# Kernel optimization log

Hardware: AMD Instinct MI355X
Metric: run time of the kernel (lower is better)

## Reference

```python
import jax, jax.numpy as jnp
import numpy as np

B, T, D_MODEL = 1, 2048, 2048
N_HEADS, N_KV_HEADS, HEAD_DIM = 32, 8, 64
N_REP = N_HEADS // N_KV_HEADS
ROPE_THETA = 10000.0


def setup_inputs() -> dict:
    key = jax.random.key(0)
    ks = jax.random.split(key, 5)
    x = jax.random.normal(ks[0], (B, T, D_MODEL), dtype=jnp.float32)
    # rotary frequencies: complex exp stored as (cos, sin) pairs -> [T, HEAD_DIM//2, 2]
    inv_freq = 1.0 / (ROPE_THETA ** (jnp.arange(0, HEAD_DIM, 2, dtype=jnp.float32) / HEAD_DIM))
    angles = jnp.arange(T, dtype=jnp.float32)[:, None] * inv_freq[None, :]  # [T, HEAD_DIM//2]
    freqs_cis = jnp.stack([jnp.cos(angles), jnp.sin(angles)], axis=-1)  # [T, HD/2, 2]
    s = 1.0 / np.sqrt(D_MODEL)
    wq = jax.random.normal(ks[1], (D_MODEL, N_HEADS * HEAD_DIM), dtype=jnp.float32) * s
    wk = jax.random.normal(ks[2], (D_MODEL, N_KV_HEADS * HEAD_DIM), dtype=jnp.float32) * s
    wv = jax.random.normal(ks[3], (D_MODEL, N_KV_HEADS * HEAD_DIM), dtype=jnp.float32) * s
    wo = jax.random.normal(ks[4], (N_HEADS * HEAD_DIM, D_MODEL), dtype=jnp.float32) * (1.0 / np.sqrt(N_HEADS * HEAD_DIM))
    return {"x": x, "freqs_cis": freqs_cis, "wq": wq, "wk": wk, "wv": wv, "wo": wo}


def _apply_rotary(t, freqs_cis):
    # t: [B, T, H, D]; freqs_cis: [T, D//2, 2] as (cos, sin). Complex multiply.
    tr = t.astype(jnp.float32).reshape(*t.shape[:-1], -1, 2)  # [B,T,H,D/2,2]
    re, im = tr[..., 0], tr[..., 1]
    cos = freqs_cis[None, :, None, :, 0]  # [1,T,1,D/2]
    sin = freqs_cis[None, :, None, :, 1]
    out_re = re * cos - im * sin
    out_im = re * sin + im * cos
    out = jnp.stack([out_re, out_im], axis=-1).reshape(t.shape)
    return out.astype(t.dtype)


def reference(x, freqs_cis, wq, wk, wv, wo):
    Bx, Tx, _ = x.shape
    q = (x @ wq).reshape(Bx, Tx, N_HEADS, HEAD_DIM)
    k = (x @ wk).reshape(Bx, Tx, N_KV_HEADS, HEAD_DIM)
    v = (x @ wv).reshape(Bx, Tx, N_KV_HEADS, HEAD_DIM)
    q = _apply_rotary(q, freqs_cis)
    k = _apply_rotary(k, freqs_cis)
    # GQA: group query heads, broadcast against kv heads (no repeat materialization)
    qg = q.transpose(0, 2, 1, 3).reshape(Bx, N_KV_HEADS, N_REP, Tx, HEAD_DIM)  # [B,G,R,T,D]
    kg = k.transpose(0, 2, 1, 3)  # [B,G,T,D]
    vg = v.transpose(0, 2, 1, 3)  # [B,G,T,D]
    scale = 1.0 / np.sqrt(HEAD_DIM)
    scores = jnp.einsum('bgrtd,bgsd->bgrts', qg, kg) * scale  # [B,G,R,T,T]
    causal = jnp.tril(jnp.ones((Tx, Tx), dtype=bool))
    scores = jnp.where(causal, scores, jnp.finfo(scores.dtype).min)
    p = jax.nn.softmax(scores, axis=-1)
    y = jnp.einsum('bgrts,bgsd->bgrtd', p, vg)  # [B,G,R,T,D]
    y = y.reshape(Bx, N_HEADS, Tx, HEAD_DIM).transpose(0, 2, 1, 3).reshape(Bx, Tx, N_HEADS * HEAD_DIM)
    return y @ wo
```

## Files before the change

kernel.cpp:

```cpp
#include <hip/hip_runtime.h>
#include <hip/hip_bf16.h>
#include <stdint.h>
#include <stddef.h>

#define T_SEQ 2048
#define DMODEL 2048
#define NHEADS 32
#define NKV 8
#define HD 64
#define NQD (NHEADS * HD)
#define NKVD (NKV * HD)
#define QKVN (NQD + 2 * NKVD)

typedef __bf16 bf16_t;
typedef __bf16 bf16x8 __attribute__((ext_vector_type(8)));
typedef __bf16 bf16x4 __attribute__((ext_vector_type(4)));
typedef __bf16 bf16x2 __attribute__((ext_vector_type(2)));
typedef float f32x4 __attribute__((ext_vector_type(4)));

typedef __attribute__((address_space(1))) void gvoid_t;
typedef __attribute__((address_space(3))) void lvoid_t;

__device__ __forceinline__ void gload_lds16(const void* g, void* l) {
  __builtin_amdgcn_global_load_lds((gvoid_t*)g, (lvoid_t*)l, 16, 0, 0);
}

__global__ __launch_bounds__(256) void cast_f32_bf16_kernel(
    const float* __restrict__ in, bf16_t* __restrict__ out, int n8) {
  int i = blockIdx.x * 256 + threadIdx.x;
  if (i >= n8) return;
  const float4* p = (const float4*)in + (size_t)i * 2;
  float4 a = p[0], b = p[1];
  bf16x8 o = {(bf16_t)a.x, (bf16_t)a.y, (bf16_t)a.z, (bf16_t)a.w,
              (bf16_t)b.x, (bf16_t)b.y, (bf16_t)b.z, (bf16_t)b.w};
  *(bf16x8*)(out + (size_t)i * 8) = o;
}

__global__ __launch_bounds__(256) void transpose_cast_kernel(
    const float* __restrict__ in, bf16_t* __restrict__ out,
    int R, int C, int ldin, int ldout) {
  __shared__ float tile[32][33];
  const int c0 = blockIdx.x * 32, r0 = blockIdx.y * 32;
  const int tx = threadIdx.x & 31, ty = threadIdx.x >> 5;
#pragma unroll
  for (int i = 0; i < 32; i += 8)
    tile[ty + i][tx] = in[(size_t)(r0 + ty + i) * ldin + c0 + tx];
  __syncthreads();
#pragma unroll
  for (int i = 0; i < 32; i += 8)
    out[(size_t)(c0 + ty + i) * ldout + r0 + tx] = (bf16_t)tile[tx][ty + i];
}

__global__ __launch_bounds__(256) void rope_cast_kernel(
    const float* __restrict__ src, const float* __restrict__ fc,
    bf16_t* __restrict__ dst, int H, int ldin, float oscale) {
  const int i = blockIdx.x * 256 + threadIdx.x;
  const int npr = H * 32;
  const int t = i / npr;
  const int rem = i - t * npr;
  const int h = rem >> 5, fi = rem & 31;
  const float2 rein = *(const float2*)&src[(size_t)t * ldin + h * 64 + fi * 2];
  const float2 cs = *(const float2*)&fc[((size_t)t * 32 + fi) * 2];
  const float o0 = (rein.x * cs.x - rein.y * cs.y) * oscale;
  const float o1 = (rein.x * cs.y + rein.y * cs.x) * oscale;
  bf16x2 ob = {(bf16_t)o0, (bf16_t)o1};
  *(bf16x2*)&dst[(size_t)t * (H * 64) + h * 64 + fi * 2] = ob;
}

__global__ __launch_bounds__(256) void gemm_bt64_kernel(
    const bf16_t* __restrict__ A, const bf16_t* __restrict__ BT,
    float* __restrict__ C, int M, int N, int K) {
  __shared__ bf16_t As[2][128 * 64];
  __shared__ bf16_t Bs[2][64 * 64];
  const int tid = threadIdx.x;
  const int lane = tid & 63;
  const int w = tid >> 6;
  const int lr = lane & 15, lg = lane >> 4;
  const int m0 = blockIdx.y * 128, n0 = blockIdx.x * 64;
  const int wm = (w >> 1) * 64, wn = (w & 1) * 32;

  const bf16_t* gA[4];
  int lAo[4];
#pragma unroll
  for (int j = 0; j < 4; ++j) {
    const int c = tid + j * 256;
    const int row = c >> 3, cc = c & 7;
    gA[j] = A + (size_t)(m0 + row) * K + ((cc ^ (row & 7)) * 8);
    lAo[j] = c * 8;
  }
  const bf16_t* gB[2];
  int lBo[2];
#pragma unroll
  for (int j = 0; j < 2; ++j) {
    const int c = tid + j * 256;
    const int row = c >> 3, cc = c & 7;
    gB[j] = BT + (size_t)(n0 + row) * K + ((cc ^ (row & 7)) * 8);
    lBo[j] = c * 8;
  }

  f32x4 acc[4][2] = {};

#pragma unroll
  for (int j = 0; j < 4; ++j) gload_lds16(gA[j], &As[0][lAo[j]]);
#pragma unroll
  for (int j = 0; j < 2; ++j) gload_lds16(gB[j], &Bs[0][lBo[j]]);
  __syncthreads();

  int cur = 0;
  for (int k0 = 0; k0 < K; k0 += 64) {
    if (k0 + 64 < K) {
#pragma unroll
      for (int j = 0; j < 4; ++j) gload_lds16(gA[j] + k0 + 64, &As[cur ^ 1][lAo[j]]);
#pragma unroll
      for (int j = 0; j < 2; ++j) gload_lds16(gB[j] + k0 + 64, &Bs[cur ^ 1][lBo[j]]);
    }
    const char* Ab = (const char*)&As[cur][0];
    const char* Bb = (const char*)&Bs[cur][0];
#pragma unroll
    for (int ks = 0; ks < 2; ++ks) {
      bf16x8 af[4], bfr[2];
#pragma unroll
      for (int mi = 0; mi < 4; ++mi) {
        const int row = wm + mi * 16 + lr;
        af[mi] = *(const bf16x8*)(Ab + row * 128 +
                                  ((ks * 64 + lg * 16) ^ ((row & 7) << 4)));
      }
#pragma unroll
      for (int nj = 0; nj < 2; ++nj) {
        const int row = wn + nj * 16 + lr;
        bfr[nj] = *(const bf16x8*)(Bb + row * 128 +
                                   ((ks * 64 + lg * 16) ^ ((row & 7) << 4)));
      }
      __builtin_amdgcn_s_setprio(1);
#pragma unroll
      for (int mi = 0; mi < 4; ++mi)
#pragma unroll
        for (int nj = 0; nj < 2; ++nj)
          acc[mi][nj] = __builtin_amdgcn_mfma_f32_16x16x32_bf16(
              af[mi], bfr[nj], acc[mi][nj], 0, 0, 0);
      __builtin_amdgcn_s_setprio(0);
    }
    __syncthreads();
    cur ^= 1;
  }

#pragma unroll
  for (int mi = 0; mi < 4; ++mi)
#pragma unroll
    for (int nj = 0; nj < 2; ++nj) {
      const int row = m0 + wm + mi * 16 + lg * 4;
      const int col = n0 + wn + nj * 16 + lr;
#pragma unroll
      for (int r = 0; r < 4; ++r)
        C[(size_t)(row + r) * N + col] = acc[mi][nj][r];
    }
}

__global__ __launch_bounds__(256) void attn_kernel(
    const bf16_t* __restrict__ Q, const bf16_t* __restrict__ Kb,
    const bf16_t* __restrict__ VT, bf16_t* __restrict__ Y,
    bf16_t* __restrict__ Yp, float* __restrict__ Lb) {
  __shared__ bf16_t Ks[2][64 * 64];
  __shared__ char Pb[4][32 * 128];
  const int bid = blockIdx.x;
  const int kh = bid & 7;
  const int item = bid >> 3;
  int qt, c, nc;
  if (item < 75) { qt = 63 - item / 3; c = item % 3; nc = 3; }
  else if (item < 115) { const int j = item - 75; qt = 38 - (j >> 1); c = j & 1; nc = 2; }
  else { qt = 18 - (item - 115); c = 0; nc = 1; }
  const int nt = (qt + 2) >> 1;
  const int tstart = (nt * c) / nc;
  const int tend = (nt * (c + 1)) / nc;
  const bool single = (nc == 1);

  const int tid = threadIdx.x, lane = tid & 63, w = tid >> 6;
  const int h = kh * 4 + w;
  const int lr = lane & 15, lg = lane >> 4;
  const int q0 = qt * 32;
  char* pb = (char*)Pb[w];
  const int swz = (lr & 7) << 4;

  const int r1 = tid >> 3, cc1 = tid & 7;
  const int r2 = r1 + 32;
  const bf16_t* kg1 = Kb + (size_t)r1 * NKVD + kh * HD + ((cc1 ^ (r1 & 7)) * 8);
  const bf16_t* kg2 = Kb + (size_t)r2 * NKVD + kh * HD + ((cc1 ^ (r2 & 7)) * 8);
  const int ld1 = tid * 8, ld2 = tid * 8 + 2048;
  const size_t kstep = (size_t)64 * NKVD;

  const bf16_t* vp0 = VT + (size_t)(kh * HD + 0 + lr) * T_SEQ + lg * 8 + tstart * 64;
  const bf16_t* vp1 = VT + (size_t)(kh * HD + 16 + lr) * T_SEQ + lg * 8 + tstart * 64;
  const bf16_t* vp2 = VT + (size_t)(kh * HD + 32 + lr) * T_SEQ + lg * 8 + tstart * 64;
  const bf16_t* vp3 = VT + (size_t)(kh * HD + 48 + lr) * T_SEQ + lg * 8 + tstart * 64;

  bf16x8 qf[2][2];
#pragma unroll
  for (int iq = 0; iq < 2; ++iq)
#pragma unroll
    for (int ks = 0; ks < 2; ++ks)
      qf[iq][ks] = *(const bf16x8*)&Q[(size_t)(q0 + iq * 16 + lr) * NQD + h * HD + ks * 32 + lg * 8];

  float l_i[2] = {0.f, 0.f};
  f32x4 acc_o[2][4] = {};
  const f32x4 Z = {0.f, 0.f, 0.f, 0.f};

  size_t koff = (size_t)tstart * kstep;
  gload_lds16(kg1 + koff, &Ks[0][ld1]);
  gload_lds16(kg2 + koff, &Ks[0][ld2]);
  __syncthreads();

  int cur = 0;
  for (int t = tstart; t < tend; ++t) {
    const int s0 = t * 64;
    if (t + 1 < tend) {
      gload_lds16(kg1 + koff + kstep, &Ks[cur ^ 1][ld1]);
      gload_lds16(kg2 + koff + kstep, &Ks[cur ^ 1][ld2]);
    }
    koff += kstep;

    bf16x8 vf[2][4];
#pragma unroll
    for (int ks = 0; ks < 2; ++ks) {
      vf[ks][0] = *(const bf16x8*)(vp0 + ks * 32);
      vf[ks][1] = *(const bf16x8*)(vp1 + ks * 32);
      vf[ks][2] = *(const bf16x8*)(vp2 + ks * 32);
      vf[ks][3] = *(const bf16x8*)(vp3 + ks * 32);
    }
    vp0 += 64; vp1 += 64; vp2 += 64; vp3 += 64;

    const char* kbase = (const char*)&Ks[cur][0];
    bf16x8 kf[4][2];
#pragma unroll
    for (int j = 0; j < 4; ++j)
#pragma unroll
      for (int ks = 0; ks < 2; ++ks)
        kf[j][ks] = *(const bf16x8*)(kbase + (j * 16 + lr) * 128 + ((ks * 64 + lg * 16) ^ swz));

    f32x4 st[2][4];
    __builtin_amdgcn_s_setprio(1);
#pragma unroll
    for (int iq = 0; iq < 2; ++iq)
#pragma unroll
      for (int j = 0; j < 4; ++j) {
        st[iq][j] = __builtin_amdgcn_mfma_f32_16x16x32_bf16(kf[j][0], qf[iq][0], Z, 0, 0, 0);
        st[iq][j] = __builtin_amdgcn_mfma_f32_16x16x32_bf16(kf[j][1], qf[iq][1], st[iq][j], 0, 0, 0);
      }
    __builtin_amdgcn_s_setprio(0);

    const bool domask = (s0 + 64 > q0);
    bf16x8 pa[2][2];
#pragma unroll
    for (int iq = 0; iq < 2; ++iq) {
      const int tq = q0 + iq * 16 + lr;
      float rs0 = 0.f, rs1 = 0.f;
      bf16_t pe[16];
      if (domask) {
#pragma unroll
        for (int j = 0; j < 4; ++j)
#pragma unroll
          for (int r = 0; r < 4; ++r) {
            const int z = j * 4 + r;
            float v = st[iq][j][r];
            if (s0 + j * 16 + lg * 4 + r > tq) v = -1e30f;
            const float p = exp2f(v);
            if (z < 8) rs0 += p; else rs1 += p;
            pe[z] = (bf16_t)p;
          }
      } else {
#pragma unroll
        for (int j = 0; j < 4; ++j)
#pragma unroll
          for (int r = 0; r < 4; ++r) {
            const int z = j * 4 + r;
            const float p = exp2f(st[iq][j][r]);
            if (z < 8) rs0 += p; else rs1 += p;
            pe[z] = (bf16_t)p;
          }
      }
      l_i[iq] += rs0 + rs1;

#pragma unroll
      for (int j = 0; j < 4; ++j) {
        bf16x4 pk = {pe[j * 4 + 0], pe[j * 4 + 1], pe[j * 4 + 2], pe[j * 4 + 3]};
        *(bf16x4*)(pb + (iq * 16 + lr) * 128 + ((j * 32 + lg * 8) ^ swz)) = pk;
      }
#pragma unroll
      for (int ks = 0; ks < 2; ++ks)
        pa[iq][ks] = *(const bf16x8*)(pb + (iq * 16 + lr) * 128 + ((ks * 64 + lg * 16) ^ swz));
    }

    __builtin_amdgcn_s_setprio(1);
#pragma unroll
    for (int iq = 0; iq < 2; ++iq)
#pragma unroll
      for (int df = 0; df < 4; ++df)
#pragma unroll
        for (int ks = 0; ks < 2; ++ks)
          acc_o[iq][df] = __builtin_amdgcn_mfma_f32_16x16x32_bf16(pa[iq][ks], vf[ks][df], acc_o[iq][df], 0, 0, 0);
    __builtin_amdgcn_s_setprio(0);

    __syncthreads();
    cur ^= 1;
  }

  float lts[2];
#pragma unroll
  for (int iq = 0; iq < 2; ++iq) {
    float lt = l_i[iq];
    lt += __shfl_xor(lt, 16);
    lt += __shfl_xor(lt, 32);
    lts[iq] = lt;
  }
  if (single) {
#pragma unroll
    for (int iq = 0; iq < 2; ++iq) {
      float lf[4];
#pragma unroll
      for (int r = 0; r < 4; ++r) lf[r] = __shfl(lts[iq], lg * 4 + r);
#pragma unroll
      for (int r = 0; r < 4; ++r) {
        const float inv = 1.f / lf[r];
        const int t = q0 + iq * 16 + lg * 4 + r;
#pragma unroll
        for (int df = 0; df < 4; ++df)
          Y[(size_t)t * NQD + h * HD + df * 16 + lr] = (bf16_t)(acc_o[iq][df][r] * inv);
      }
    }
  } else {
    const int cid = (nc == 3) ? (kh * 115 + 40 + (qt - 39) * 3 + c)
                              : (kh * 115 + (qt - 19) * 2 + c);
    bf16_t* yp = Yp + ((size_t)cid * 4 + w) * 2048;
#pragma unroll
    for (int iq = 0; iq < 2; ++iq) {
      float lf[4];
#pragma unroll
      for (int r = 0; r < 4; ++r) lf[r] = __shfl(lts[iq], lg * 4 + r);
#pragma unroll
      for (int r = 0; r < 4; ++r) {
        const float inv = 1.f / lf[r];
        const int q = iq * 16 + lg * 4 + r;
#pragma unroll
        for (int df = 0; df < 4; ++df)
          yp[q * 64 + df * 16 + lr] = (bf16_t)(acc_o[iq][df][r] * inv);
      }
    }
    if (lg == 0) {
#pragma unroll
      for (int iq = 0; iq < 2; ++iq)
        Lb[cid * 128 + w * 32 + iq * 16 + lr] = lts[iq];
    }
  }
}

__global__ __launch_bounds__(256) void merge_kernel(
    const bf16_t* __restrict__ Yp, const float* __restrict__ Lb,
    bf16_t* __restrict__ Y) {
  const int qt = 19 + blockIdx.x, kh = blockIdx.y;
  const int w = threadIdx.x >> 6, lane = threadIdx.x & 63;
  const int h = kh * 4 + w;
  const int nc = (qt < 39) ? 2 : 3;
  const int base = (qt < 39) ? (kh * 115 + (qt - 19) * 2)
                             : (kh * 115 + 40 + (qt - 39) * 3);
  const bf16_t* y0 = Yp + ((size_t)(base + 0) * 4 + w) * 2048;
  const bf16_t* y1 = Yp + ((size_t)(base + 1) * 4 + w) * 2048;
  const bf16_t* y2 = Yp + ((size_t)(base + 2) * 4 + w) * 2048;
#pragma unroll 4
  for (int q = 0; q < 32; ++q) {
    const float l0 = Lb[(base + 0) * 128 + w * 32 + q];
    const float l1 = Lb[(base + 1) * 128 + w * 32 + q];
    const float l2 = (nc == 3) ? Lb[(base + 2) * 128 + w * 32 + q] : 0.f;
    const float inv = 1.f / (l0 + l1 + l2);
    float v = (float)y0[q * 64 + lane] * l0 + (float)y1[q * 64 + lane] * l1;
    if (nc == 3) v += (float)y2[q * 64 + lane] * l2;
    Y[(size_t)(qt * 32 + q) * NQD + h * HD + lane] = (bf16_t)(v * inv);
  }
}

extern "C" void kernel_launch(void* const* d_in, const int* in_sizes, int n_in,
                              void* d_out, int out_size, void* d_ws, size_t ws_size,
                              hipStream_t stream) {
  const float* x = (const float*)d_in[0];
  const float* fc = (const float*)d_in[1];
  const float* wq = (const float*)d_in[2];
  const float* wk = (const float*)d_in[3];
  const float* wv = (const float*)d_in[4];
  const float* wo = (const float*)d_in[5];
  float* out = (float*)d_out;
  char* ws = (char*)d_ws;

  bf16_t* xb   = (bf16_t*)(ws + 0);
  bf16_t* wT   = (bf16_t*)(ws + (8u << 20));
  float*  qkvf = (float*)(ws + (20u << 20));
  bf16_t* qb   = (bf16_t*)(ws + (8u << 20));
  bf16_t* kb   = (bf16_t*)(ws + (16u << 20));
  bf16_t* vt   = (bf16_t*)(ws + (18u << 20));
  bf16_t* woT  = (bf16_t*)(ws + (20u << 20));
  bf16_t* yb   = (bf16_t*)(ws + 0);
  float*  Lb   = (float*)(ws + (28u << 20));
  bf16_t* Yp   = (bf16_t*)d_out;

  const float SCL_Q = 0.18033688011112042f;

  hipLaunchKernelGGL(cast_f32_bf16_kernel, dim3(2048), dim3(256), 0, stream,
                     x, xb, (T_SEQ * DMODEL) / 8);
  hipLaunchKernelGGL(transpose_cast_kernel, dim3(64, 64), dim3(256), 0, stream,
                     wq, wT, DMODEL, NQD, NQD, DMODEL);
  hipLaunchKernelGGL(transpose_cast_kernel, dim3(16, 64), dim3(256), 0, stream,
                     wk, wT + (size_t)NQD * DMODEL, DMODEL, NKVD, NKVD, DMODEL);
  hipLaunchKernelGGL(transpose_cast_kernel, dim3(16, 64), dim3(256), 0, stream,
                     wv, wT + (size_t)(NQD + NKVD) * DMODEL, DMODEL, NKVD, NKVD, DMODEL);
  hipLaunchKernelGGL(gemm_bt64_kernel, dim3(QKVN / 64, T_SEQ / 128), dim3(256), 0, stream,
                     xb, wT, qkvf, T_SEQ, QKVN, DMODEL);
  hipLaunchKernelGGL(rope_cast_kernel, dim3((T_SEQ * NHEADS * 32) / 256), dim3(256), 0, stream,
                     qkvf, fc, qb, NHEADS, QKVN, SCL_Q);
  hipLaunchKernelGGL(rope_cast_kernel, dim3((T_SEQ * NKV * 32) / 256), dim3(256), 0, stream,
                     qkvf + NQD, fc, kb, NKV, QKVN, 1.0f);
  hipLaunchKernelGGL(transpose_cast_kernel, dim3(16, 64), dim3(256), 0, stream,
                     qkvf + NQD + NKVD, vt, T_SEQ, NKVD, QKVN, T_SEQ);
  hipLaunchKernelGGL(transpose_cast_kernel, dim3(64, 64), dim3(256), 0, stream,
                     wo, woT, NQD, DMODEL, DMODEL, NQD);
  hipLaunchKernelGGL(attn_kernel, dim3(134 * 8), dim3(256), 0, stream,
                     qb, kb, vt, yb, Yp, Lb);
  hipLaunchKernelGGL(merge_kernel, dim3(45, 8), dim3(256), 0, stream,
                     Yp, Lb, yb);
  hipLaunchKernelGGL(gemm_bt64_kernel, dim3(DMODEL / 64, T_SEQ / 128), dim3(256), 0, stream,
                     yb, woT, out, T_SEQ, DMODEL, NQD);
}
```

Before: 177.9 us.

## Use 128x128 GEMM tiles with XCD-aware block mapping and bf16 QKV output

Both GEMMs move from 128x64 tiles to 128x128 tiles, so each wave computes a 64x64 block. The 1D grid is remapped so that blocks sharing the same N columns land on the same XCD. The QKV projection now writes bf16 instead of fp32, which halves the intermediate traffic read by the RoPE and V-transpose kernels. The workspace layout is reshuffled to fit. The trade-off is fewer blocks (384 and 256) on a large-CU device, so occupancy and load balance may suffer, and Q/K/V are rounded to bf16 before RoPE is applied.

```diff
diff --git a/kernel.cpp b/kernel.cpp
--- a/kernel.cpp
+++ b/kernel.cpp
@@ -36,15 +36,16 @@
   *(bf16x8*)(out + (size_t)i * 8) = o;
 }
 
+template <typename TIN>
 __global__ __launch_bounds__(256) void transpose_cast_kernel(
-    const float* __restrict__ in, bf16_t* __restrict__ out,
+    const TIN* __restrict__ in, bf16_t* __restrict__ out,
     int R, int C, int ldin, int ldout) {
   __shared__ float tile[32][33];
   const int c0 = blockIdx.x * 32, r0 = blockIdx.y * 32;
   const int tx = threadIdx.x & 31, ty = threadIdx.x >> 5;
 #pragma unroll
   for (int i = 0; i < 32; i += 8)
-    tile[ty + i][tx] = in[(size_t)(r0 + ty + i) * ldin + c0 + tx];
+    tile[ty + i][tx] = (float)in[(size_t)(r0 + ty + i) * ldin + c0 + tx];
   __syncthreads();
 #pragma unroll
   for (int i = 0; i < 32; i += 8)
@@ -52,73 +53,72 @@
 }
 
 __global__ __launch_bounds__(256) void rope_cast_kernel(
-    const float* __restrict__ src, const float* __restrict__ fc,
+    const bf16_t* __restrict__ src, const float* __restrict__ fc,
     bf16_t* __restrict__ dst, int H, int ldin, float oscale) {
   const int i = blockIdx.x * 256 + threadIdx.x;
   const int npr = H * 32;
   const int t = i / npr;
   const int rem = i - t * npr;
   const int h = rem >> 5, fi = rem & 31;
-  const float2 rein = *(const float2*)&src[(size_t)t * ldin + h * 64 + fi * 2];
+  const bf16x2 rb = *(const bf16x2*)&src[(size_t)t * ldin + h * 64 + fi * 2];
+  const float re = (float)rb[0], im = (float)rb[1];
   const float2 cs = *(const float2*)&fc[((size_t)t * 32 + fi) * 2];
-  const float o0 = (rein.x * cs.x - rein.y * cs.y) * oscale;
-  const float o1 = (rein.x * cs.y + rein.y * cs.x) * oscale;
+  const float o0 = (re * cs.x - im * cs.y) * oscale;
+  const float o1 = (re * cs.y + im * cs.x) * oscale;
   bf16x2 ob = {(bf16_t)o0, (bf16_t)o1};
   *(bf16x2*)&dst[(size_t)t * (H * 64) + h * 64 + fi * 2] = ob;
 }
 
-__global__ __launch_bounds__(256) void gemm_bt64_kernel(
+template <typename CT>
+__global__ __launch_bounds__(256) void gemm128_kernel(
     const bf16_t* __restrict__ A, const bf16_t* __restrict__ BT,
-    float* __restrict__ C, int M, int N, int K) {
+    CT* __restrict__ C, int M, int N, int K, int mt, int ncpx) {
   __shared__ bf16_t As[2][128 * 64];
-  __shared__ bf16_t Bs[2][64 * 64];
+  __shared__ bf16_t Bs[2][128 * 64];
+  const int bid = blockIdx.x;
+  const int xcd = bid & 7, idx = bid >> 3;
+  const int n0 = (xcd * ncpx + idx / mt) * 128;
+  const int m0 = (idx % mt) * 128;
   const int tid = threadIdx.x;
   const int lane = tid & 63;
   const int w = tid >> 6;
   const int lr = lane & 15, lg = lane >> 4;
-  const int m0 = blockIdx.y * 128, n0 = blockIdx.x * 64;
-  const int wm = (w >> 1) * 64, wn = (w & 1) * 32;
+  const int wm = (w >> 1) * 64, wn = (w & 1) * 64;
 
   const bf16_t* gA[4];
-  int lAo[4];
+  const bf16_t* gB[4];
+  int lo[4];
 #pragma unroll
   for (int j = 0; j < 4; ++j) {
     const int c = tid + j * 256;
     const int row = c >> 3, cc = c & 7;
-    gA[j] = A + (size_t)(m0 + row) * K + ((cc ^ (row & 7)) * 8);
-    lAo[j] = c * 8;
-  }
-  const bf16_t* gB[2];
-  int lBo[2];
-#pragma unroll
-  for (int j = 0; j < 2; ++j) {
-    const int c = tid + j * 256;
-    const int row = c >> 3, cc = c & 7;
-    gB[j] = BT + (size_t)(n0 + row) * K + ((cc ^ (row & 7)) * 8);
-    lBo[j] = c * 8;
-  }
-
-  f32x4 acc[4][2] = {};
-
-#pragma unroll
-  for (int j = 0; j < 4; ++j) gload_lds16(gA[j], &As[0][lAo[j]]);
-#pragma unroll
-  for (int j = 0; j < 2; ++j) gload_lds16(gB[j], &Bs[0][lBo[j]]);
+    const int co = (cc ^ (row & 7)) * 8;
+    gA[j] = A + (size_t)(m0 + row) * K + co;
+    gB[j] = BT + (size_t)(n0 + row) * K + co;
+    lo[j] = c * 8;
+  }
+
+  f32x4 acc[4][4] = {};
+
+#pragma unroll
+  for (int j = 0; j < 4; ++j) gload_lds16(gA[j], &As[0][lo[j]]);
+#pragma unroll
+  for (int j = 0; j < 4; ++j) gload_lds16(gB[j], &Bs[0][lo[j]]);
   __syncthreads();
 
   int cur = 0;
   for (int k0 = 0; k0 < K; k0 += 64) {
     if (k0 + 64 < K) {
 #pragma unroll
-      for (int j = 0; j < 4; ++j) gload_lds16(gA[j] + k0 + 64, &As[cur ^ 1][lAo[j]]);
-#pragma unroll
-      for (int j = 0; j < 2; ++j) gload_lds16(gB[j] + k0 + 64, &Bs[cur ^ 1][lBo[j]]);
+      for (int j = 0; j < 4; ++j) gload_lds16(gA[j] + k0 + 64, &As[cur ^ 1][lo[j]]);
+#pragma unroll
+      for (int j = 0; j < 4; ++j) gload_lds16(gB[j] + k0 + 64, &Bs[cur ^ 1][lo[j]]);
     }
     const char* Ab = (const char*)&As[cur][0];
     const char* Bb = (const char*)&Bs[cur][0];
 #pragma unroll
     for (int ks = 0; ks < 2; ++ks) {
-      bf16x8 af[4], bfr[2];
+      bf16x8 af[4], bfr[4];
 #pragma unroll
       for (int mi = 0; mi < 4; ++mi) {
         const int row = wm + mi * 16 + lr;
@@ -126,7 +126,7 @@
                                   ((ks * 64 + lg * 16) ^ ((row & 7) << 4)));
       }
 #pragma unroll
-      for (int nj = 0; nj < 2; ++nj) {
+      for (int nj = 0; nj < 4; ++nj) {
         const int row = wn + nj * 16 + lr;
         bfr[nj] = *(const bf16x8*)(Bb + row * 128 +
                                    ((ks * 64 + lg * 16) ^ ((row & 7) << 4)));
@@ -135,7 +135,7 @@
 #pragma unroll
       for (int mi = 0; mi < 4; ++mi)
 #pragma unroll
-        for (int nj = 0; nj < 2; ++nj)
+        for (int nj = 0; nj < 4; ++nj)
           acc[mi][nj] = __builtin_amdgcn_mfma_f32_16x16x32_bf16(
               af[mi], bfr[nj], acc[mi][nj], 0, 0, 0);
       __builtin_amdgcn_s_setprio(0);
@@ -147,12 +147,12 @@
 #pragma unroll
   for (int mi = 0; mi < 4; ++mi)
 #pragma unroll
-    for (int nj = 0; nj < 2; ++nj) {
+    for (int nj = 0; nj < 4; ++nj) {
       const int row = m0 + wm + mi * 16 + lg * 4;
       const int col = n0 + wn + nj * 16 + lr;
 #pragma unroll
       for (int r = 0; r < 4; ++r)
-        C[(size_t)(row + r) * N + col] = acc[mi][nj][r];
+        C[(size_t)(row + r) * N + col] = (CT)acc[mi][nj][r];
     }
 }
 
@@ -390,12 +390,12 @@
 
   bf16_t* xb   = (bf16_t*)(ws + 0);
   bf16_t* wT   = (bf16_t*)(ws + (8u << 20));
-  float*  qkvf = (float*)(ws + (20u << 20));
-  bf16_t* qb   = (bf16_t*)(ws + (8u << 20));
-  bf16_t* kb   = (bf16_t*)(ws + (16u << 20));
-  bf16_t* vt   = (bf16_t*)(ws + (18u << 20));
-  bf16_t* woT  = (bf16_t*)(ws + (20u << 20));
-  bf16_t* yb   = (bf16_t*)(ws + 0);
+  bf16_t* qkvb = (bf16_t*)(ws + (20u << 20));
+  bf16_t* qb   = (bf16_t*)(ws + 0);
+  bf16_t* kb   = (bf16_t*)(ws + (8u << 20));
+  bf16_t* vt   = (bf16_t*)(ws + (10u << 20));
+  bf16_t* woT  = (bf16_t*)(ws + (12u << 20));
+  bf16_t* yb   = (bf16_t*)(ws + (20u << 20));
   float*  Lb   = (float*)(ws + (28u << 20));
   bf16_t* Yp   = (bf16_t*)d_out;
 
@@ -403,26 +403,26 @@
 
   hipLaunchKernelGGL(cast_f32_bf16_kernel, dim3(2048), dim3(256), 0, stream,
                      x, xb, (T_SEQ * DMODEL) / 8);
-  hipLaunchKernelGGL(transpose_cast_kernel, dim3(64, 64), dim3(256), 0, stream,
+  hipLaunchKernelGGL(transpose_cast_kernel<float>, dim3(64, 64), dim3(256), 0, stream,
                      wq, wT, DMODEL, NQD, NQD, DMODEL);
-  hipLaunchKernelGGL(transpose_cast_kernel, dim3(16, 64), dim3(256), 0, stream,
+  hipLaunchKernelGGL(transpose_cast_kernel<float>, dim3(16, 64), dim3(256), 0, stream,
                      wk, wT + (size_t)NQD * DMODEL, DMODEL, NKVD, NKVD, DMODEL);
-  hipLaunchKernelGGL(transpose_cast_kernel, dim3(16, 64), dim3(256), 0, stream,
+  hipLaunchKernelGGL(transpose_cast_kernel<float>, dim3(16, 64), dim3(256), 0, stream,
                      wv, wT + (size_t)(NQD + NKVD) * DMODEL, DMODEL, NKVD, NKVD, DMODEL);
-  hipLaunchKernelGGL(gemm_bt64_kernel, dim3(QKVN / 64, T_SEQ / 128), dim3(256), 0, stream,
-                     xb, wT, qkvf, T_SEQ, QKVN, DMODEL);
+  hipLaunchKernelGGL(gemm128_kernel<bf16_t>, dim3(384), dim3(256), 0, stream,
+                     xb, wT, qkvb, T_SEQ, QKVN, DMODEL, T_SEQ / 128, (QKVN / 128) / 8);
   hipLaunchKernelGGL(rope_cast_kernel, dim3((T_SEQ * NHEADS * 32) / 256), dim3(256), 0, stream,
-                     qkvf, fc, qb, NHEADS, QKVN, SCL_Q);
+                     qkvb, fc, qb, NHEADS, QKVN, SCL_Q);
   hipLaunchKernelGGL(rope_cast_kernel, dim3((T_SEQ * NKV * 32) / 256), dim3(256), 0, stream,
-                     qkvf + NQD, fc, kb, NKV, QKVN, 1.0f);
-  hipLaunchKernelGGL(transpose_cast_kernel, dim3(16, 64), dim3(256), 0, stream,
-                     qkvf + NQD + NKVD, vt, T_SEQ, NKVD, QKVN, T_SEQ);
-  hipLaunchKernelGGL(transpose_cast_kernel, dim3(64, 64), dim3(256), 0, stream,
+                     qkvb + NQD, fc, kb, NKV, QKVN, 1.0f);
+  hipLaunchKernelGGL(transpose_cast_kernel<bf16_t>, dim3(16, 64), dim3(256), 0, stream,
+                     qkvb + NQD + NKVD, vt, T_SEQ, NKVD, QKVN, T_SEQ);
+  hipLaunchKernelGGL(transpose_cast_kernel<float>, dim3(64, 64), dim3(256), 0, stream,
                      wo, woT, NQD, DMODEL, DMODEL, NQD);
   hipLaunchKernelGGL(attn_kernel, dim3(134 * 8), dim3(256), 0, stream,
                      qb, kb, vt, yb, Yp, Lb);
   hipLaunchKernelGGL(merge_kernel, dim3(45, 8), dim3(256), 0, stream,
                      Yp, Lb, yb);
-  hipLaunchKernelGGL(gemm_bt64_kernel, dim3(DMODEL / 64, T_SEQ / 128), dim3(256), 0, stream,
-                     yb, woT, out, T_SEQ, DMODEL, NQD);
-}
+  hipLaunchKernelGGL(gemm128_kernel<float>, dim3(256), dim3(256), 0, stream,
+                     yb, woT, out, T_SEQ, DMODEL, NQD, T_SEQ / 128, (DMODEL / 128) / 8);
+}
```

Measured after the change: 193.8 us. +8.9%, slower.

## Store QKV projection in bf16 and load K directly from global in attention

Applied to the files above, without the earlier changes.

The QKV GEMM now writes a bf16 intermediate instead of fp32, which halves the write and read traffic for the rope and V-transpose kernels, and the workspace layout is rearranged to fit. The attention kernel drops its LDS double-buffered K staging and block barriers, and each wave loads K fragments straight from global memory (through cache) the same way V is loaded. This removes the syncthreads and LDS traffic but gives up the shared reuse of K across the four waves. It also adds an extra bf16 rounding before RoPE.

```diff
diff --git a/kernel.cpp b/kernel.cpp
--- a/kernel.cpp
+++ b/kernel.cpp
@@ -36,15 +36,16 @@
   *(bf16x8*)(out + (size_t)i * 8) = o;
 }
 
+template <typename TIN>
 __global__ __launch_bounds__(256) void transpose_cast_kernel(
-    const float* __restrict__ in, bf16_t* __restrict__ out,
+    const TIN* __restrict__ in, bf16_t* __restrict__ out,
     int R, int C, int ldin, int ldout) {
   __shared__ float tile[32][33];
   const int c0 = blockIdx.x * 32, r0 = blockIdx.y * 32;
   const int tx = threadIdx.x & 31, ty = threadIdx.x >> 5;
 #pragma unroll
   for (int i = 0; i < 32; i += 8)
-    tile[ty + i][tx] = in[(size_t)(r0 + ty + i) * ldin + c0 + tx];
+    tile[ty + i][tx] = (float)in[(size_t)(r0 + ty + i) * ldin + c0 + tx];
   __syncthreads();
 #pragma unroll
   for (int i = 0; i < 32; i += 8)
@@ -52,24 +53,26 @@
 }
 
 __global__ __launch_bounds__(256) void rope_cast_kernel(
-    const float* __restrict__ src, const float* __restrict__ fc,
+    const bf16_t* __restrict__ src, const float* __restrict__ fc,
     bf16_t* __restrict__ dst, int H, int ldin, float oscale) {
   const int i = blockIdx.x * 256 + threadIdx.x;
   const int npr = H * 32;
   const int t = i / npr;
   const int rem = i - t * npr;
   const int h = rem >> 5, fi = rem & 31;
-  const float2 rein = *(const float2*)&src[(size_t)t * ldin + h * 64 + fi * 2];
+  const bf16x2 rb = *(const bf16x2*)&src[(size_t)t * ldin + h * 64 + fi * 2];
+  const float re = (float)rb[0], im = (float)rb[1];
   const float2 cs = *(const float2*)&fc[((size_t)t * 32 + fi) * 2];
-  const float o0 = (rein.x * cs.x - rein.y * cs.y) * oscale;
-  const float o1 = (rein.x * cs.y + rein.y * cs.x) * oscale;
+  const float o0 = (re * cs.x - im * cs.y) * oscale;
+  const float o1 = (re * cs.y + im * cs.x) * oscale;
   bf16x2 ob = {(bf16_t)o0, (bf16_t)o1};
   *(bf16x2*)&dst[(size_t)t * (H * 64) + h * 64 + fi * 2] = ob;
 }
 
+template <typename CT>
 __global__ __launch_bounds__(256) void gemm_bt64_kernel(
     const bf16_t* __restrict__ A, const bf16_t* __restrict__ BT,
-    float* __restrict__ C, int M, int N, int K) {
+    CT* __restrict__ C, int M, int N, int K) {
   __shared__ bf16_t As[2][128 * 64];
   __shared__ bf16_t Bs[2][64 * 64];
   const int tid = threadIdx.x;
@@ -152,7 +155,7 @@
       const int col = n0 + wn + nj * 16 + lr;
 #pragma unroll
       for (int r = 0; r < 4; ++r)
-        C[(size_t)(row + r) * N + col] = acc[mi][nj][r];
+        C[(size_t)(row + r) * N + col] = (CT)acc[mi][nj][r];
     }
 }
 
@@ -160,7 +163,6 @@
     const bf16_t* __restrict__ Q, const bf16_t* __restrict__ Kb,
     const bf16_t* __restrict__ VT, bf16_t* __restrict__ Y,
     bf16_t* __restrict__ Yp, float* __restrict__ Lb) {
-  __shared__ bf16_t Ks[2][64 * 64];
   __shared__ char Pb[4][32 * 128];
   const int bid = blockIdx.x;
   const int kh = bid & 7;
@@ -181,12 +183,7 @@
   char* pb = (char*)Pb[w];
   const int swz = (lr & 7) << 4;
 
-  const int r1 = tid >> 3, cc1 = tid & 7;
-  const int r2 = r1 + 32;
-  const bf16_t* kg1 = Kb + (size_t)r1 * NKVD + kh * HD + ((cc1 ^ (r1 & 7)) * 8);
-  const bf16_t* kg2 = Kb + (size_t)r2 * NKVD + kh * HD + ((cc1 ^ (r2 & 7)) * 8);
-  const int ld1 = tid * 8, ld2 = tid * 8 + 2048;
-  const size_t kstep = (size_t)64 * NKVD;
+  const bf16_t* kp = Kb + (size_t)(tstart * 64 + lr) * NKVD + kh * HD + lg * 8;
 
   const bf16_t* vp0 = VT + (size_t)(kh * HD + 0 + lr) * T_SEQ + lg * 8 + tstart * 64;
   const bf16_t* vp1 = VT + (size_t)(kh * HD + 16 + lr) * T_SEQ + lg * 8 + tstart * 64;
@@ -204,19 +201,15 @@
   f32x4 acc_o[2][4] = {};
   const f32x4 Z = {0.f, 0.f, 0.f, 0.f};
 
-  size_t koff = (size_t)tstart * kstep;
-  gload_lds16(kg1 + koff, &Ks[0][ld1]);
-  gload_lds16(kg2 + koff, &Ks[0][ld2]);
-  __syncthreads();
-
-  int cur = 0;
   for (int t = tstart; t < tend; ++t) {
     const int s0 = t * 64;
-    if (t + 1 < tend) {
-      gload_lds16(kg1 + koff + kstep, &Ks[cur ^ 1][ld1]);
-      gload_lds16(kg2 + koff + kstep, &Ks[cur ^ 1][ld2]);
-    }
-    koff += kstep;
+
+    bf16x8 kf[4][2];
+#pragma unroll
+    for (int j = 0; j < 4; ++j)
+#pragma unroll
+      for (int ks = 0; ks < 2; ++ks)
+        kf[j][ks] = *(const bf16x8*)(kp + (size_t)j * 16 * NKVD + ks * 32);
 
     bf16x8 vf[2][4];
 #pragma unroll
@@ -226,15 +219,8 @@
       vf[ks][2] = *(const bf16x8*)(vp2 + ks * 32);
       vf[ks][3] = *(const bf16x8*)(vp3 + ks * 32);
     }
+    kp += (size_t)64 * NKVD;
     vp0 += 64; vp1 += 64; vp2 += 64; vp3 += 64;
-
-    const char* kbase = (const char*)&Ks[cur][0];
-    bf16x8 kf[4][2];
-#pragma unroll
-    for (int j = 0; j < 4; ++j)
-#pragma unroll
-      for (int ks = 0; ks < 2; ++ks)
-        kf[j][ks] = *(const bf16x8*)(kbase + (j * 16 + lr) * 128 + ((ks * 64 + lg * 16) ^ swz));
 
     f32x4 st[2][4];
     __builtin_amdgcn_s_setprio(1);
@@ -298,9 +284,6 @@
         for (int ks = 0; ks < 2; ++ks)
           acc_o[iq][df] = __builtin_amdgcn_mfma_f32_16x16x32_bf16(pa[iq][ks], vf[ks][df], acc_o[iq][df], 0, 0, 0);
     __builtin_amdgcn_s_setprio(0);
-
-    __syncthreads();
-    cur ^= 1;
   }
 
   float lts[2];
@@ -390,12 +373,12 @@
 
   bf16_t* xb   = (bf16_t*)(ws + 0);
   bf16_t* wT   = (bf16_t*)(ws + (8u << 20));
-  float*  qkvf = (float*)(ws + (20u << 20));
-  bf16_t* qb   = (bf16_t*)(ws + (8u << 20));
-  bf16_t* kb   = (bf16_t*)(ws + (16u << 20));
-  bf16_t* vt   = (bf16_t*)(ws + (18u << 20));
-  bf16_t* woT  = (bf16_t*)(ws + (20u << 20));
-  bf16_t* yb   = (bf16_t*)(ws + 0);
+  bf16_t* qkvb = (bf16_t*)(ws + (20u << 20));
+  bf16_t* qb   = (bf16_t*)(ws + 0);
+  bf16_t* kb   = (bf16_t*)(ws + (8u << 20));
+  bf16_t* vt   = (bf16_t*)(ws + (10u << 20));
+  bf16_t* woT  = (bf16_t*)(ws + (12u << 20));
+  bf16_t* yb   = (bf16_t*)(ws + (20u << 20));
   float*  Lb   = (float*)(ws + (28u << 20));
   bf16_t* Yp   = (bf16_t*)d_out;
 
@@ -403,26 +386,26 @@
 
   hipLaunchKernelGGL(cast_f32_bf16_kernel, dim3(2048), dim3(256), 0, stream,
                      x, xb, (T_SEQ * DMODEL) / 8);
-  hipLaunchKernelGGL(transpose_cast_kernel, dim3(64, 64), dim3(256), 0, stream,
+  hipLaunchKernelGGL(transpose_cast_kernel<float>, dim3(64, 64), dim3(256), 0, stream,
                      wq, wT, DMODEL, NQD, NQD, DMODEL);
-  hipLaunchKernelGGL(transpose_cast_kernel, dim3(16, 64), dim3(256), 0, stream,
+  hipLaunchKernelGGL(transpose_cast_kernel<float>, dim3(16, 64), dim3(256), 0, stream,
                      wk, wT + (size_t)NQD * DMODEL, DMODEL, NKVD, NKVD, DMODEL);
-  hipLaunchKernelGGL(transpose_cast_kernel, dim3(16, 64), dim3(256), 0, stream,
+  hipLaunchKernelGGL(transpose_cast_kernel<float>, dim3(16, 64), dim3(256), 0, stream,
                      wv, wT + (size_t)(NQD + NKVD) * DMODEL, DMODEL, NKVD, NKVD, DMODEL);
-  hipLaunchKernelGGL(gemm_bt64_kernel, dim3(QKVN / 64, T_SEQ / 128), dim3(256), 0, stream,
-                     xb, wT, qkvf, T_SEQ, QKVN, DMODEL);
+  hipLaunchKernelGGL(gemm_bt64_kernel<bf16_t>, dim3(QKVN / 64, T_SEQ / 128), dim3(256), 0, stream,
+                     xb, wT, qkvb, T_SEQ, QKVN, DMODEL);
   hipLaunchKernelGGL(rope_cast_kernel, dim3((T_SEQ * NHEADS * 32) / 256), dim3(256), 0, stream,
-                     qkvf, fc, qb, NHEADS, QKVN, SCL_Q);
+                     qkvb, fc, qb, NHEADS, QKVN, SCL_Q);
   hipLaunchKernelGGL(rope_cast_kernel, dim3((T_SEQ * NKV * 32) / 256), dim3(256), 0, stream,
-                     qkvf + NQD, fc, kb, NKV, QKVN, 1.0f);
-  hipLaunchKernelGGL(transpose_cast_kernel, dim3(16, 64), dim3(256), 0, stream,
-                     qkvf + NQD + NKVD, vt, T_SEQ, NKVD, QKVN, T_SEQ);
-  hipLaunchKernelGGL(transpose_cast_kernel, dim3(64, 64), dim3(256), 0, stream,
+                     qkvb + NQD, fc, kb, NKV, QKVN, 1.0f);
+  hipLaunchKernelGGL(transpose_cast_kernel<bf16_t>, dim3(16, 64), dim3(256), 0, stream,
+                     qkvb + NQD + NKVD, vt, T_SEQ, NKVD, QKVN, T_SEQ);
+  hipLaunchKernelGGL(transpose_cast_kernel<float>, dim3(64, 64), dim3(256), 0, stream,
                      wo, woT, NQD, DMODEL, DMODEL, NQD);
   hipLaunchKernelGGL(attn_kernel, dim3(134 * 8), dim3(256), 0, stream,
                      qb, kb, vt, yb, Yp, Lb);
   hipLaunchKernelGGL(merge_kernel, dim3(45, 8), dim3(256), 0, stream,
                      Yp, Lb, yb);
-  hipLaunchKernelGGL(gemm_bt64_kernel, dim3(DMODEL / 64, T_SEQ / 128), dim3(256), 0, stream,
+  hipLaunchKernelGGL(gemm_bt64_kernel<float>, dim3(DMODEL / 64, T_SEQ / 128), dim3(256), 0, stream,
                      yb, woT, out, T_SEQ, DMODEL, NQD);
 }
```

New measurement: 196.9 us. 1.11x slower.
